# Kernel optimization log

Hardware: AMD Instinct MI355X
Metric: run time of the kernel (lower is better)

The kernel has to match this reference:

```python
import jax, jax.numpy as jnp
import numpy as np

B, D, H, K, P = 16384, 64, 256, 8, 3  # batch, lattice dim, hidden, expressivity, num_pars


def setup_inputs() -> dict:
    key = jax.random.key(0)
    k0, k1, k2 = jax.random.split(key, 3)
    # U(1) angles in [0, 2*pi)
    z = jax.random.uniform(k0, (B, D), dtype=jnp.float32) * (2.0 * jnp.pi)
    # per-step conditioner MLP weights, padded to full input dim (causally masked in reference)
    W1 = jax.random.normal(k1, (D - 1, D, H), dtype=jnp.float32) * 0.05
    b1 = jnp.zeros((D - 1, H), dtype=jnp.float32)
    W2 = jax.random.normal(k2, (D - 1, H, P * K), dtype=jnp.float32) * 0.05
    b2 = jnp.zeros((D - 1, P * K), dtype=jnp.float32)
    return {"z": z, "W1": W1, "b1": b1, "W2": W2, "b2": b2}


def reference(z, W1, b1, W2, b2):
    # decode(): x[...,0]=0; for idx in 1..D-1:
    #   params = conditioner_idx(z[..., :idx]); x[..., idx], ld = diffeo(z[..., idx], *params)
    # All conditioners read only z, so steps are independent -> vectorize over steps.
    d = z.shape[-1]
    r = d - 1
    # mask[row, col] = col < row+1  (conditioner idx uses first idx inputs)
    mask = (jnp.arange(d)[None, :] < (jnp.arange(r) + 1)[:, None]).astype(z.dtype)  # [R, D]
    W1m = W1 * mask[:, :, None]                                   # causal zero-padding
    h = jax.nn.relu(jnp.einsum('bd,rdh->brh', z, W1m) + b1)       # [B, R, H]
    raw = jnp.einsum('brh,rhp->brp', h, W2) + b2                  # [B, R, 3K]
    a_u, b_u, r_u = jnp.split(raw, 3, axis=-1)                    # each [B, R, K]
    alpha = jnp.exp(a_u)
    beta = b_u
    rho = jax.nn.softmax(r_u, axis=-1)
    # NCP diffeomorphism on U(1): convex mixture of 2*atan(alpha*tan((z-pi)/2)+beta)+pi
    zi = z[:, 1:]                                                  # [B, R]
    t = jnp.tan((zi - jnp.pi) * 0.5)[..., None]                    # [B, R, 1]
    g = alpha * t + beta                                           # [B, R, K]
    x_tail = jnp.sum(rho * (2.0 * jnp.arctan(g) + jnp.pi), axis=-1)
    deriv = alpha * (1.0 + t * t) / (1.0 + g * g)                  # dh/dz per component
    ld = jnp.log(jnp.sum(rho * deriv, axis=-1))                    # [B, R]
    x = jnp.concatenate([jnp.zeros_like(z[:, :1]), x_tail], axis=-1)
    log_det = jnp.sum(ld, axis=-1)                                 # [B]
    return x, log_det
```

## Files before the change

### kernel.cpp

```cpp
#include <hip/hip_runtime.h>
#include <math.h>
#include <type_traits>

typedef __bf16 bf16x8 __attribute__((ext_vector_type(8)));
typedef float f32x4 __attribute__((ext_vector_type(4)));
typedef unsigned int u32x4 __attribute__((ext_vector_type(4)));

#define B_TOT 16384
#define D_TOT 64
#define R_TOT 63
#define H_TOT 256
#define PK_TOT 24
#define PI_F 3.14159265358979323846f

#define W2F_BASE_U32 516096u
#define WS_NEED 3096576u

#define MFMA16(a, b, c) __builtin_amdgcn_mfma_f32_16x16x32_bf16((a), (b), (c), 0, 0, 0)

__device__ __forceinline__ unsigned short bf16_rtne(float f) {
    unsigned u = __float_as_uint(f);
    unsigned rr = u + 0x7FFFu + ((u >> 16) & 1u);
    return (unsigned short)(rr >> 16);
}

__device__ __forceinline__ unsigned cvt_pk_bf16(float a, float b) {
    unsigned r;
    asm("v_cvt_pk_bf16_f32 %0, %1, %2" : "=v"(r) : "v"(a), "v"(b));
    return r;
}

__global__ void init_out_kernel(float* __restrict__ out) {
    int b = blockIdx.x * 256 + threadIdx.x;
    if (b < B_TOT) {
        out[(size_t)b * D_TOT] = 0.0f;
        out[(size_t)B_TOT * D_TOT + b] = 0.0f;
    }
}

__global__ void prep_weights(const float* __restrict__ W1,
                             const float* __restrict__ b1,
                             const float* __restrict__ W2,
                             unsigned int* __restrict__ wsf)
{
    int gid = blockIdx.x * 256 + threadIdx.x;
    if (gid >= 193536) return;
    float v[8];
    unsigned int* dst;
    if (gid < 129024) {
        int lane = gid & 63;
        int q = gid >> 6;
        int t = q & 1; int qq = q >> 1;
        int nt = qq & 15; int r = qq >> 4;
        int n  = (nt << 4) + (lane & 15);
        int kb = (t << 5) + ((lane >> 4) << 3);
        int bias_d = (r <= 30) ? 31 : 63;
        #pragma unroll
        for (int j = 0; j < 8; ++j) {
            int d = kb + j;
            v[j] = (d <= r) ? W1[(size_t)(r * 64 + d) * 256 + n]
                 : (d == bias_d ? b1[(size_t)r * 256 + n] : 0.0f);
        }
        dst = wsf + (size_t)q * 256 + ((unsigned)lane << 2);
    } else {
        int g2 = gid - 129024;
        int lane = g2 & 63;
        int q = g2 >> 6;
        int ks = q & 7; int qq = q >> 3;
        int nt = qq & 1; int r = qq >> 1;
        int n  = (nt << 4) + (lane & 15);
        int kb = (ks << 5) + ((lane >> 4) << 3);
        #pragma unroll
        for (int j = 0; j < 8; ++j) {
            int k = kb + j;
            v[j] = (n < PK_TOT) ? W2[(size_t)(r * 256 + k) * PK_TOT + n] : 0.0f;
        }
        dst = wsf + W2F_BASE_U32 + (size_t)q * 256 + ((unsigned)lane << 2);
    }
    unsigned hw[4];
    #pragma unroll
    for (int i = 0; i < 4; ++i)
        hw[i] = (unsigned)bf16_rtne(v[2 * i]) | ((unsigned)bf16_rtne(v[2 * i + 1]) << 16);
    *reinterpret_cast<u32x4*>(dst) = u32x4{hw[0], hw[1], hw[2], hw[3]};
}

__global__ __launch_bounds__(256, 4) void flow_mfma(
    const float* __restrict__ z, const unsigned int* __restrict__ wsf,
    const float* __restrict__ b2, float* __restrict__ out)
{
    const int r   = blockIdx.y;
    const int b0  = blockIdx.x << 6;
    const int tid = threadIdx.x;
    const int w   = tid >> 6;
    const int l   = tid & 63;
    const int l15 = l & 15, l4 = l >> 4, key = l & 7;

    __shared__ __align__(16) unsigned char sm[24832];
    float* tls = reinterpret_cast<float*>(sm + 24576);

    {
        const int m  = tid >> 2;
        const int dq = (tid & 3) << 4;
        const float* zp = z + (size_t)(b0 + m) * 64 + dq;
        const int mkey = m & 7;
        const int bias_d = (r <= 30) ? 31 : 63;
        const int rel = bias_d - dq;
        const int tel = (r + 1) - dq;
        #pragma unroll
        for (int qq = 0; qq < 4; ++qq) {
            float4 val = *reinterpret_cast<const float4*>(zp + (qq << 2));
            int d0 = dq + (qq << 2);
            float vv[4] = {val.x, val.y, val.z, val.w};
            if ((tel >> 2) == qq) {
                float zi = vv[tel & 3];
                float s, c;
                __sincosf(zi * 0.5f, &s, &c);
                float t = -c * __builtin_amdgcn_rcpf(s);
                tls[m] = fminf(fmaxf(t, -1e8f), 1e8f);
            }
            if ((rel >> 2) == qq) vv[rel & 3] = 1.0f;
            uint2 hv;
            hv.x = cvt_pk_bf16(vv[0], vv[1]);
            hv.y = cvt_pk_bf16(vv[2], vv[3]);
            int off = (m << 7) + ((((d0 >> 3)) ^ mkey) << 4) + (((d0 >> 2) & 1) << 3);
            *reinterpret_cast<uint2*>(sm + off) = hv;
        }
    }
    __syncthreads();

    const unsigned int* w1b = wsf + (size_t)((r * 16 + (w << 2)) * 2) * 256 + (l << 2);
    const unsigned int* w2b = wsf + W2F_BASE_U32 + (size_t)(r * 16) * 256 + (l << 2);

    const int ej  = tid & 7;
    const float b2a = b2[(size_t)r * 24 + ej];
    const float b2b = b2[(size_t)r * 24 + 8 + ej];
    const float b2r = b2[(size_t)r * 24 + 16 + ej];

    #pragma unroll 1
    for (int mh = 0; mh < 2; ++mh) {
        f32x4 acc1[4][2];
        #pragma unroll
        for (int a = 0; a < 4; ++a)
            #pragma unroll
            for (int b = 0; b < 2; ++b) acc1[a][b] = f32x4{0.f, 0.f, 0.f, 0.f};

        auto run_gemm1 = [&](auto FULLC) {
            constexpr int NT = decltype(FULLC)::value ? 2 : 1;
            #pragma unroll
            for (int t = 0; t < NT; ++t) {
                bf16x8 zf[2];
                #pragma unroll
                for (int mt = 0; mt < 2; ++mt) {
                    int m = (mh << 5) + (mt << 4) + l15;
                    int off = (m << 7) + ((((t << 2) + l4) ^ key) << 4);
                    zf[mt] = __builtin_bit_cast(bf16x8, *reinterpret_cast<u32x4*>(sm + off));
                }
                #pragma unroll
                for (int ntl = 0; ntl < 4; ++ntl) {
                    bf16x8 af = __builtin_bit_cast(bf16x8,
                        *reinterpret_cast<const u32x4*>(w1b + (((ntl << 1) + t) << 8)));
                    #pragma unroll
                    for (int mt = 0; mt < 2; ++mt)
                        acc1[ntl][mt] = MFMA16(af, zf[mt], acc1[ntl][mt]);
                }
            }
        };
        if (r >= 31) run_gemm1(std::true_type{});
        else         run_gemm1(std::false_type{});

        #pragma unroll
        for (int ntl = 0; ntl < 4; ++ntl) {
            #pragma unroll
            for (int mt = 0; mt < 2; ++mt) {
                float v0 = fmaxf(acc1[ntl][mt][0], 0.0f);
                float v1 = fmaxf(acc1[ntl][mt][1], 0.0f);
                float v2 = fmaxf(acc1[ntl][mt][2], 0.0f);
                float v3 = fmaxf(acc1[ntl][mt][3], 0.0f);
                uint2 hv;
                hv.x = cvt_pk_bf16(v0, v1);
                hv.y = cvt_pk_bf16(v2, v3);
                int mloc = (mt << 4) + l15;
                int g    = (w << 3) + (ntl << 1) + (l4 >> 1);
                int off  = 8192 + (mloc << 9)
                         + (((g & 24) | ((g ^ key) & 7)) << 4) + ((l4 & 1) << 3);
                *reinterpret_cast<uint2*>(sm + off) = hv;
            }
        }
        __syncthreads();

        f32x4 acc2[2][2];
        #pragma unroll
        for (int a = 0; a < 2; ++a)
            #pragma unroll
            for (int b = 0; b < 2; ++b) acc2[a][b] = f32x4{0.f, 0.f, 0.f, 0.f};

        #pragma unroll
        for (int kk = 0; kk < 2; ++kk) {
            const int ks = (w << 1) + kk;
            bf16x8 wf[2];
            #pragma unroll
            for (int nt2 = 0; nt2 < 2; ++nt2)
                wf[nt2] = __builtin_bit_cast(bf16x8,
                    *reinterpret_cast<const u32x4*>(w2b + (((nt2 << 3) + ks) << 8)));
            bf16x8 hfr[2];
            #pragma unroll
            for (int mt = 0; mt < 2; ++mt) {
                int mloc = (mt << 4) + l15;
                int g    = (ks << 2) + l4;
                int off  = 8192 + (mloc << 9)
                         + (((g & 24) | ((g ^ key) & 7)) << 4);
                hfr[mt] = __builtin_bit_cast(bf16x8, *reinterpret_cast<u32x4*>(sm + off));
            }
            #pragma unroll
            for (int nt2 = 0; nt2 < 2; ++nt2)
                #pragma unroll
                for (int mt = 0; mt < 2; ++mt)
                    acc2[nt2][mt] = MFMA16(wf[nt2], hfr[mt], acc2[nt2][mt]);
        }
        __syncthreads();

        #pragma unroll
        for (int nt2 = 0; nt2 < 2; ++nt2)
            #pragma unroll
            for (int mt = 0; mt < 2; ++mt) {
                int row = (w << 5) + (mt << 4) + l15;
                int off = 8192 + (row << 7) + ((((nt2 << 2) + l4) ^ key) << 4);
                *reinterpret_cast<f32x4*>(sm + off) = acc2[nt2][mt];
            }
        __syncthreads();

        {
            const int mloc = tid >> 3;
            const int j    = ej;
            const int mk   = mloc & 7;
            float ra = b2a, rb = b2b, rr = b2r;
            #pragma unroll
            for (int w4 = 0; w4 < 4; ++w4) {
                const int base = 8192 + (((w4 << 5) + mloc) << 7);
                const int sub  = (j & 3) << 2;
                ra += *reinterpret_cast<float*>(sm + base + ((((j) >> 2) ^ mk) << 4) + sub);
                rb += *reinterpret_cast<float*>(sm + base + (((2 + (j >> 2)) ^ mk) << 4) + sub);
                rr += *reinterpret_cast<float*>(sm + base + (((4 + (j >> 2)) ^ mk) << 4) + sub);
            }
            int gb = b0 + (mh << 5) + mloc;
            float t  = tls[(mh << 5) + mloc];
            float al = __expf(ra);
            float g  = fmaf(al, t, rb);
            float X  = 2.0f * atanf(g) + PI_F;
            float dv = al * fmaf(t, t, 1.0f) * __builtin_amdgcn_rcpf(fmaf(g, g, 1.0f));
            float mx = rr;
            mx = fmaxf(mx, __shfl_xor(mx, 1));
            mx = fmaxf(mx, __shfl_xor(mx, 2));
            mx = fmaxf(mx, __shfl_xor(mx, 4));
            float e = __expf(rr - mx);
            float se = e, sx = e * X, sd = e * dv;
            se += __shfl_xor(se, 1); se += __shfl_xor(se, 2); se += __shfl_xor(se, 4);
            sx += __shfl_xor(sx, 1); sx += __shfl_xor(sx, 2); sx += __shfl_xor(sx, 4);
            sd += __shfl_xor(sd, 1); sd += __shfl_xor(sd, 2); sd += __shfl_xor(sd, 4);
            if (j == 0) {
                float rse = __builtin_amdgcn_rcpf(se);
                out[(size_t)gb * D_TOT + r + 1] = sx * rse;
                atomicAdd(&out[(size_t)B_TOT * D_TOT + gb], __logf(sd * rse));
            }
        }
        __syncthreads();
    }
}

__global__ __launch_bounds__(256, 2) void flow_fp32(
    const float* __restrict__ z,  const float* __restrict__ W1,
    const float* __restrict__ b1, const float* __restrict__ W2,
    const float* __restrict__ b2, float* __restrict__ out)
{
    const int r   = blockIdx.y;
    const int b0  = blockIdx.x * 32;
    const int tid = threadIdx.x;

    __shared__ float smem[16384];
    float* z_t  = smem;
    float* h_s  = smem + 2048;
    float* w2t  = smem + 2048 + 8192;
    float* part = w2t;

    #pragma unroll
    for (int it = 0; it < 2; ++it) {
        int idx4 = it * 256 + tid;
        int brow = idx4 >> 4;
        int dq   = (idx4 & 15) << 2;
        float4 v = *reinterpret_cast<const float4*>(&z[(size_t)(b0 + brow) * D_TOT + dq]);
        z_t[(dq + 0) * 32 + brow] = v.x;
        z_t[(dq + 1) * 32 + brow] = v.y;
        z_t[(dq + 2) * 32 + brow] = v.z;
        z_t[(dq + 3) * 32 + brow] = v.w;
    }
    #pragma unroll
    for (int it = 0; it < 6; ++it) {
        int idx4 = it * 256 + tid;
        int k  = idx4 / 6;
        int pq = (idx4 - k * 6) << 2;
        float4 v = *reinterpret_cast<const float4*>(&W2[(size_t)(r * H_TOT + k) * PK_TOT + pq]);
        int gk = k >> 2, kq = k & 3;
        w2t[(pq + 0) * 256 + (((gk) ^ ((pq + 0) & 7)) << 2) + kq] = v.x;
        w2t[(pq + 1) * 256 + (((gk) ^ ((pq + 1) & 7)) << 2) + kq] = v.y;
        w2t[(pq + 2) * 256 + (((gk) ^ ((pq + 2) & 7)) << 2) + kq] = v.z;
        w2t[(pq + 3) * 256 + (((gk) ^ ((pq + 3) & 7)) << 2) + kq] = v.w;
    }
    __syncthreads();

    const int rg = tid & 15;
    const int cg = tid >> 4;
    float acc[2][16];
    #pragma unroll
    for (int j = 0; j < 2; ++j)
        #pragma unroll
        for (int i = 0; i < 16; ++i) acc[j][i] = 0.0f;

    const float* w1p = W1 + (size_t)(r * D_TOT) * H_TOT + (cg << 4);
    #pragma unroll 4
    for (int d = 0; d <= r; ++d) {
        float2 zv = *reinterpret_cast<const float2*>(&z_t[d * 32 + (rg << 1)]);
        const float* wrow = w1p + (size_t)d * H_TOT;
        float wv[16];
        *reinterpret_cast<float4*>(&wv[0])  = *reinterpret_cast<const float4*>(wrow + 0);
        *reinterpret_cast<float4*>(&wv[4])  = *reinterpret_cast<const float4*>(wrow + 4);
        *reinterpret_cast<float4*>(&wv[8])  = *reinterpret_cast<const float4*>(wrow + 8);
        *reinterpret_cast<float4*>(&wv[12]) = *reinterpret_cast<const float4*>(wrow + 12);
        #pragma unroll
        for (int i = 0; i < 16; ++i) {
            acc[0][i] = fmaf(zv.x, wv[i], acc[0][i]);
            acc[1][i] = fmaf(zv.y, wv[i], acc[1][i]);
        }
    }
    {
        const int key = (rg >> 1) & 7;
        #pragma unroll
        for (int gi = 0; gi < 4; ++gi) {
            float4 bv = *reinterpret_cast<const float4*>(&b1[(size_t)r * H_TOT + (cg << 4) + (gi << 2)]);
            #pragma unroll
            for (int j = 0; j < 2; ++j) {
                float4 v;
                v.x = fmaxf(acc[j][4 * gi + 0] + bv.x, 0.0f);
                v.y = fmaxf(acc[j][4 * gi + 1] + bv.y, 0.0f);
                v.z = fmaxf(acc[j][4 * gi + 2] + bv.z, 0.0f);
                v.w = fmaxf(acc[j][4 * gi + 3] + bv.w, 0.0f);
                int bb = (rg << 1) + j;
                int g  = ((cg << 2) + gi) ^ key;
                *reinterpret_cast<float4*>(&h_s[bb * 256 + (g << 2)]) = v;
            }
        }
    }
    __syncthreads();

    const int wv_ = tid >> 6;
    const int ln  = tid & 63;
    const int bq  = ln & 7;
    const int pg  = ln >> 3;
    float acc2[4][3];
    #pragma unroll
    for (int j = 0; j < 4; ++j)
        #pragma unroll
        for (int i = 0; i < 3; ++i) acc2[j][i] = 0.0f;

    #pragma unroll
    for (int c = 0; c < 8; ++c) {
        int k0  = (wv_ << 6) + (c << 3);
        int gk0 = k0 >> 2;
        float w2r[3][8], hr[4][8];
        #pragma unroll
        for (int i = 0; i < 3; ++i) {
            int p = 3 * pg + i, pk = p & 7;
            *reinterpret_cast<float4*>(&w2r[i][0]) =
                *reinterpret_cast<const float4*>(&w2t[p * 256 + (((gk0 + 0) ^ pk) << 2)]);
            *reinterpret_cast<float4*>(&w2r[i][4]) =
                *reinterpret_cast<const float4*>(&w2t[p * 256 + (((gk0 + 1) ^ pk) << 2)]);
        }
        #pragma unroll
        for (int j = 0; j < 4; ++j) {
            int bb = 4 * bq + j;
            *reinterpret_cast<float4*>(&hr[j][0]) =
                *reinterpret_cast<const float4*>(&h_s[bb * 256 + (((gk0 + 0) ^ bq) << 2)]);
            *reinterpret_cast<float4*>(&hr[j][4]) =
                *reinterpret_cast<const float4*>(&h_s[bb * 256 + (((gk0 + 1) ^ bq) << 2)]);
        }
        #pragma unroll
        for (int kk = 0; kk < 8; ++kk)
            #pragma unroll
            for (int j = 0; j < 4; ++j)
                #pragma unroll
                for (int i = 0; i < 3; ++i)
                    acc2[j][i] = fmaf(hr[j][kk], w2r[i][kk], acc2[j][i]);
    }
    __syncthreads();
    #pragma unroll
    for (int j = 0; j < 4; ++j)
        #pragma unroll
        for (int i = 0; i < 3; ++i)
            part[((wv_ << 5) + 4 * bq + j) * PK_TOT + 3 * pg + i] = acc2[j][i];
    __syncthreads();

    {
        const int eb = tid >> 3;
        const int ej = tid & 7;
        float rawa = b2[(size_t)r * PK_TOT + ej];
        float rawb = b2[(size_t)r * PK_TOT + 8 + ej];
        float rawr = b2[(size_t)r * PK_TOT + 16 + ej];
        #pragma unroll
        for (int w = 0; w < 4; ++w) {
            rawa += part[((w << 5) + eb) * PK_TOT + ej];
            rawb += part[((w << 5) + eb) * PK_TOT + 8 + ej];
            rawr += part[((w << 5) + eb) * PK_TOT + 16 + ej];
        }
        float zi = z_t[(r + 1) * 32 + eb];
        float t  = tanf((zi - PI_F) * 0.5f);
        float al = expf(rawa);
        float g  = fmaf(al, t, rawb);
        float X  = 2.0f * atanf(g) + PI_F;
        float dv = al * (1.0f + t * t) / (1.0f + g * g);
        float m = rawr;
        m = fmaxf(m, __shfl_xor(m, 1));
        m = fmaxf(m, __shfl_xor(m, 2));
        m = fmaxf(m, __shfl_xor(m, 4));
        float e  = expf(rawr - m);
        float se = e, sx = e * X, sd = e * dv;
        se += __shfl_xor(se, 1); se += __shfl_xor(se, 2); se += __shfl_xor(se, 4);
        sx += __shfl_xor(sx, 1); sx += __shfl_xor(sx, 2); sx += __shfl_xor(sx, 4);
        sd += __shfl_xor(sd, 1); sd += __shfl_xor(sd, 2); sd += __shfl_xor(sd, 4);
        if (ej == 0) {
            int gb = b0 + eb;
            out[(size_t)gb * D_TOT + (r + 1)] = sx / se;
            atomicAdd(&out[(size_t)B_TOT * D_TOT + gb], logf(sd / se));
        }
    }
}

extern "C" void kernel_launch(void* const* d_in, const int* in_sizes, int n_in,
                              void* d_out, int out_size, void* d_ws, size_t ws_size,
                              hipStream_t stream) {
    const float* z  = (const float*)d_in[0];
    const float* W1 = (const float*)d_in[1];
    const float* b1 = (const float*)d_in[2];
    const float* W2 = (const float*)d_in[3];
    const float* b2 = (const float*)d_in[4];
    float* out = (float*)d_out;

    init_out_kernel<<<dim3(B_TOT / 256), dim3(256), 0, stream>>>(out);
    if (ws_size >= (size_t)WS_NEED) {
        prep_weights<<<dim3(756), dim3(256), 0, stream>>>(W1, b1, W2, (unsigned int*)d_ws);
        flow_mfma<<<dim3(B_TOT / 64, R_TOT), dim3(256), 0, stream>>>(
            z, (const unsigned int*)d_ws, b2, out);
    } else {
        flow_fp32<<<dim3(B_TOT / 32, R_TOT), dim3(256), 0, stream>>>(z, W1, b1, W2, b2, out);
    }
}
```

Measured before the change: 111.0 us.

## Process two conditioner steps per block to reuse staged z and batch log-det atomics

Each block now handles two steps r (paired so both share the same bias column and K-extent class), halving the grid along the step axis. The z tile is loaded and converted to bf16 once per pair, and the log-det contributions are accumulated in registers and written with one atomic per row per block instead of one per step. The cost is fewer blocks, a longer serial loop per block, and slightly more shared memory for the second t array.

After: 103.5 us. -6.8%, faster.

```diff
diff --git a/kernel.cpp b/kernel.cpp
--- a/kernel.cpp
+++ b/kernel.cpp
@@ -88,14 +88,20 @@
     const float* __restrict__ z, const unsigned int* __restrict__ wsf,
     const float* __restrict__ b2, float* __restrict__ out)
 {
-    const int r   = blockIdx.y;
+    const int y   = blockIdx.y;
+    int r0, r1;
+    if (y < 15)       { r0 = 2 * y;     r1 = 2 * y + 1; }
+    else if (y == 15) { r0 = 30;        r1 = -1;        }
+    else              { r0 = 2 * y - 1; r1 = 2 * y;     }
+    const int bias_d = (y <= 15) ? 31 : 63;
+
     const int b0  = blockIdx.x << 6;
     const int tid = threadIdx.x;
     const int w   = tid >> 6;
     const int l   = tid & 63;
     const int l15 = l & 15, l4 = l >> 4, key = l & 7;
 
-    __shared__ __align__(16) unsigned char sm[24832];
+    __shared__ __align__(16) unsigned char sm[25088];
     float* tls = reinterpret_cast<float*>(sm + 24576);
 
     {
@@ -103,20 +109,27 @@
         const int dq = (tid & 3) << 4;
         const float* zp = z + (size_t)(b0 + m) * 64 + dq;
         const int mkey = m & 7;
-        const int bias_d = (r <= 30) ? 31 : 63;
-        const int rel = bias_d - dq;
-        const int tel = (r + 1) - dq;
+        const int rel  = bias_d - dq;
+        const int tel0 = (r0 + 1) - dq;
+        const int tel1 = (r1 + 1) - dq;
         #pragma unroll
         for (int qq = 0; qq < 4; ++qq) {
             float4 val = *reinterpret_cast<const float4*>(zp + (qq << 2));
             int d0 = dq + (qq << 2);
             float vv[4] = {val.x, val.y, val.z, val.w};
-            if ((tel >> 2) == qq) {
-                float zi = vv[tel & 3];
+            if ((tel0 >> 2) == qq) {
+                float zi = vv[tel0 & 3];
                 float s, c;
                 __sincosf(zi * 0.5f, &s, &c);
                 float t = -c * __builtin_amdgcn_rcpf(s);
                 tls[m] = fminf(fmaxf(t, -1e8f), 1e8f);
+            }
+            if ((tel1 >> 2) == qq) {
+                float zi = vv[tel1 & 3];
+                float s, c;
+                __sincosf(zi * 0.5f, &s, &c);
+                float t = -c * __builtin_amdgcn_rcpf(s);
+                tls[64 + m] = fminf(fmaxf(t, -1e8f), 1e8f);
             }
             if ((rel >> 2) == qq) vv[rel & 3] = 1.0f;
             uint2 hv;
@@ -128,142 +141,156 @@
     }
     __syncthreads();
 
-    const unsigned int* w1b = wsf + (size_t)((r * 16 + (w << 2)) * 2) * 256 + (l << 2);
-    const unsigned int* w2b = wsf + W2F_BASE_U32 + (size_t)(r * 16) * 256 + (l << 2);
-
-    const int ej  = tid & 7;
-    const float b2a = b2[(size_t)r * 24 + ej];
-    const float b2b = b2[(size_t)r * 24 + 8 + ej];
-    const float b2r = b2[(size_t)r * 24 + 16 + ej];
+    const int ej = tid & 7;
+    float ld0 = 0.0f, ld1 = 0.0f;
 
     #pragma unroll 1
-    for (int mh = 0; mh < 2; ++mh) {
-        f32x4 acc1[4][2];
-        #pragma unroll
-        for (int a = 0; a < 4; ++a)
-            #pragma unroll
-            for (int b = 0; b < 2; ++b) acc1[a][b] = f32x4{0.f, 0.f, 0.f, 0.f};
-
-        auto run_gemm1 = [&](auto FULLC) {
-            constexpr int NT = decltype(FULLC)::value ? 2 : 1;
-            #pragma unroll
-            for (int t = 0; t < NT; ++t) {
-                bf16x8 zf[2];
+    for (int ri = 0; ri < 2; ++ri) {
+        const int r = ri ? r1 : r0;
+        if (r < 0) break;
+
+        const unsigned int* w1b = wsf + (size_t)((r * 16 + (w << 2)) * 2) * 256 + (l << 2);
+        const unsigned int* w2b = wsf + W2F_BASE_U32 + (size_t)(r * 16) * 256 + (l << 2);
+        const float b2a = b2[(size_t)r * 24 + ej];
+        const float b2b = b2[(size_t)r * 24 + 8 + ej];
+        const float b2r = b2[(size_t)r * 24 + 16 + ej];
+
+        #pragma unroll 1
+        for (int mh = 0; mh < 2; ++mh) {
+            f32x4 acc1[4][2];
+            #pragma unroll
+            for (int a = 0; a < 4; ++a)
+                #pragma unroll
+                for (int b = 0; b < 2; ++b) acc1[a][b] = f32x4{0.f, 0.f, 0.f, 0.f};
+
+            auto run_gemm1 = [&](auto FULLC) {
+                constexpr int NT = decltype(FULLC)::value ? 2 : 1;
+                #pragma unroll
+                for (int t = 0; t < NT; ++t) {
+                    bf16x8 zf[2];
+                    #pragma unroll
+                    for (int mt = 0; mt < 2; ++mt) {
+                        int m = (mh << 5) + (mt << 4) + l15;
+                        int off = (m << 7) + ((((t << 2) + l4) ^ key) << 4);
+                        zf[mt] = __builtin_bit_cast(bf16x8, *reinterpret_cast<u32x4*>(sm + off));
+                    }
+                    #pragma unroll
+                    for (int ntl = 0; ntl < 4; ++ntl) {
+                        bf16x8 af = __builtin_bit_cast(bf16x8,
+                            *reinterpret_cast<const u32x4*>(w1b + (((ntl << 1) + t) << 8)));
+                        #pragma unroll
+                        for (int mt = 0; mt < 2; ++mt)
+                            acc1[ntl][mt] = MFMA16(af, zf[mt], acc1[ntl][mt]);
+                    }
+                }
+            };
+            if (r >= 31) run_gemm1(std::true_type{});
+            else         run_gemm1(std::false_type{});
+
+            #pragma unroll
+            for (int ntl = 0; ntl < 4; ++ntl) {
                 #pragma unroll
                 for (int mt = 0; mt < 2; ++mt) {
-                    int m = (mh << 5) + (mt << 4) + l15;
-                    int off = (m << 7) + ((((t << 2) + l4) ^ key) << 4);
-                    zf[mt] = __builtin_bit_cast(bf16x8, *reinterpret_cast<u32x4*>(sm + off));
-                }
-                #pragma unroll
-                for (int ntl = 0; ntl < 4; ++ntl) {
-                    bf16x8 af = __builtin_bit_cast(bf16x8,
-                        *reinterpret_cast<const u32x4*>(w1b + (((ntl << 1) + t) << 8)));
+                    float v0 = fmaxf(acc1[ntl][mt][0], 0.0f);
+                    float v1 = fmaxf(acc1[ntl][mt][1], 0.0f);
+                    float v2 = fmaxf(acc1[ntl][mt][2], 0.0f);
+                    float v3 = fmaxf(acc1[ntl][mt][3], 0.0f);
+                    uint2 hv;
+                    hv.x = cvt_pk_bf16(v0, v1);
+                    hv.y = cvt_pk_bf16(v2, v3);
+                    int mloc = (mt << 4) + l15;
+                    int g    = (w << 3) + (ntl << 1) + (l4 >> 1);
+                    int off  = 8192 + (mloc << 9)
+                             + (((g & 24) | ((g ^ key) & 7)) << 4) + ((l4 & 1) << 3);
+                    *reinterpret_cast<uint2*>(sm + off) = hv;
+                }
+            }
+            __syncthreads();
+
+            f32x4 acc2[2][2];
+            #pragma unroll
+            for (int a = 0; a < 2; ++a)
+                #pragma unroll
+                for (int b = 0; b < 2; ++b) acc2[a][b] = f32x4{0.f, 0.f, 0.f, 0.f};
+
+            #pragma unroll
+            for (int kk = 0; kk < 2; ++kk) {
+                const int ks = (w << 1) + kk;
+                bf16x8 wf[2];
+                #pragma unroll
+                for (int nt2 = 0; nt2 < 2; ++nt2)
+                    wf[nt2] = __builtin_bit_cast(bf16x8,
+                        *reinterpret_cast<const u32x4*>(w2b + (((nt2 << 3) + ks) << 8)));
+                bf16x8 hfr[2];
+                #pragma unroll
+                for (int mt = 0; mt < 2; ++mt) {
+                    int mloc = (mt << 4) + l15;
+                    int g    = (ks << 2) + l4;
+                    int off  = 8192 + (mloc << 9)
+                             + (((g & 24) | ((g ^ key) & 7)) << 4);
+                    hfr[mt] = __builtin_bit_cast(bf16x8, *reinterpret_cast<u32x4*>(sm + off));
+                }
+                #pragma unroll
+                for (int nt2 = 0; nt2 < 2; ++nt2)
                     #pragma unroll
                     for (int mt = 0; mt < 2; ++mt)
-                        acc1[ntl][mt] = MFMA16(af, zf[mt], acc1[ntl][mt]);
-                }
-            }
-        };
-        if (r >= 31) run_gemm1(std::true_type{});
-        else         run_gemm1(std::false_type{});
-
-        #pragma unroll
-        for (int ntl = 0; ntl < 4; ++ntl) {
-            #pragma unroll
-            for (int mt = 0; mt < 2; ++mt) {
-                float v0 = fmaxf(acc1[ntl][mt][0], 0.0f);
-                float v1 = fmaxf(acc1[ntl][mt][1], 0.0f);
-                float v2 = fmaxf(acc1[ntl][mt][2], 0.0f);
-                float v3 = fmaxf(acc1[ntl][mt][3], 0.0f);
-                uint2 hv;
-                hv.x = cvt_pk_bf16(v0, v1);
-                hv.y = cvt_pk_bf16(v2, v3);
-                int mloc = (mt << 4) + l15;
-                int g    = (w << 3) + (ntl << 1) + (l4 >> 1);
-                int off  = 8192 + (mloc << 9)
-                         + (((g & 24) | ((g ^ key) & 7)) << 4) + ((l4 & 1) << 3);
-                *reinterpret_cast<uint2*>(sm + off) = hv;
-            }
-        }
-        __syncthreads();
-
-        f32x4 acc2[2][2];
-        #pragma unroll
-        for (int a = 0; a < 2; ++a)
-            #pragma unroll
-            for (int b = 0; b < 2; ++b) acc2[a][b] = f32x4{0.f, 0.f, 0.f, 0.f};
-
-        #pragma unroll
-        for (int kk = 0; kk < 2; ++kk) {
-            const int ks = (w << 1) + kk;
-            bf16x8 wf[2];
+                        acc2[nt2][mt] = MFMA16(wf[nt2], hfr[mt], acc2[nt2][mt]);
+            }
+            __syncthreads();
+
             #pragma unroll
             for (int nt2 = 0; nt2 < 2; ++nt2)
-                wf[nt2] = __builtin_bit_cast(bf16x8,
-                    *reinterpret_cast<const u32x4*>(w2b + (((nt2 << 3) + ks) << 8)));
-            bf16x8 hfr[2];
-            #pragma unroll
-            for (int mt = 0; mt < 2; ++mt) {
-                int mloc = (mt << 4) + l15;
-                int g    = (ks << 2) + l4;
-                int off  = 8192 + (mloc << 9)
-                         + (((g & 24) | ((g ^ key) & 7)) << 4);
-                hfr[mt] = __builtin_bit_cast(bf16x8, *reinterpret_cast<u32x4*>(sm + off));
-            }
-            #pragma unroll
-            for (int nt2 = 0; nt2 < 2; ++nt2)
-                #pragma unroll
-                for (int mt = 0; mt < 2; ++mt)
-                    acc2[nt2][mt] = MFMA16(wf[nt2], hfr[mt], acc2[nt2][mt]);
-        }
-        __syncthreads();
-
-        #pragma unroll
-        for (int nt2 = 0; nt2 < 2; ++nt2)
-            #pragma unroll
-            for (int mt = 0; mt < 2; ++mt) {
-                int row = (w << 5) + (mt << 4) + l15;
-                int off = 8192 + (row << 7) + ((((nt2 << 2) + l4) ^ key) << 4);
-                *reinterpret_cast<f32x4*>(sm + off) = acc2[nt2][mt];
-            }
-        __syncthreads();
-
-        {
-            const int mloc = tid >> 3;
-            const int j    = ej;
-            const int mk   = mloc & 7;
-            float ra = b2a, rb = b2b, rr = b2r;
-            #pragma unroll
-            for (int w4 = 0; w4 < 4; ++w4) {
-                const int base = 8192 + (((w4 << 5) + mloc) << 7);
-                const int sub  = (j & 3) << 2;
-                ra += *reinterpret_cast<float*>(sm + base + ((((j) >> 2) ^ mk) << 4) + sub);
-                rb += *reinterpret_cast<float*>(sm + base + (((2 + (j >> 2)) ^ mk) << 4) + sub);
-                rr += *reinterpret_cast<float*>(sm + base + (((4 + (j >> 2)) ^ mk) << 4) + sub);
-            }
-            int gb = b0 + (mh << 5) + mloc;
-            float t  = tls[(mh << 5) + mloc];
-            float al = __expf(ra);
-            float g  = fmaf(al, t, rb);
-            float X  = 2.0f * atanf(g) + PI_F;
-            float dv = al * fmaf(t, t, 1.0f) * __builtin_amdgcn_rcpf(fmaf(g, g, 1.0f));
-            float mx = rr;
-            mx = fmaxf(mx, __shfl_xor(mx, 1));
-            mx = fmaxf(mx, __shfl_xor(mx, 2));
-            mx = fmaxf(mx, __shfl_xor(mx, 4));
-            float e = __expf(rr - mx);
-            float se = e, sx = e * X, sd = e * dv;
-            se += __shfl_xor(se, 1); se += __shfl_xor(se, 2); se += __shfl_xor(se, 4);
-            sx += __shfl_xor(sx, 1); sx += __shfl_xor(sx, 2); sx += __shfl_xor(sx, 4);
-            sd += __shfl_xor(sd, 1); sd += __shfl_xor(sd, 2); sd += __shfl_xor(sd, 4);
-            if (j == 0) {
-                float rse = __builtin_amdgcn_rcpf(se);
-                out[(size_t)gb * D_TOT + r + 1] = sx * rse;
-                atomicAdd(&out[(size_t)B_TOT * D_TOT + gb], __logf(sd * rse));
-            }
-        }
-        __syncthreads();
+                #pragma unroll
+                for (int mt = 0; mt < 2; ++mt) {
+                    int row = (w << 5) + (mt << 4) + l15;
+                    int off = 8192 + (row << 7) + ((((nt2 << 2) + l4) ^ key) << 4);
+                    *reinterpret_cast<f32x4*>(sm + off) = acc2[nt2][mt];
+                }
+            __syncthreads();
+
+            {
+                const int mloc = tid >> 3;
+                const int j    = ej;
+                const int mk   = mloc & 7;
+                float ra = b2a, rb = b2b, rr = b2r;
+                #pragma unroll
+                for (int w4 = 0; w4 < 4; ++w4) {
+                    const int base = 8192 + (((w4 << 5) + mloc) << 7);
+                    const int sub  = (j & 3) << 2;
+                    ra += *reinterpret_cast<float*>(sm + base + ((((j) >> 2) ^ mk) << 4) + sub);
+                    rb += *reinterpret_cast<float*>(sm + base + (((2 + (j >> 2)) ^ mk) << 4) + sub);
+                    rr += *reinterpret_cast<float*>(sm + base + (((4 + (j >> 2)) ^ mk) << 4) + sub);
+                }
+                int gb = b0 + (mh << 5) + mloc;
+                float t  = tls[(ri << 6) + (mh << 5) + mloc];
+                float al = __expf(ra);
+                float g  = fmaf(al, t, rb);
+                float X  = 2.0f * atanf(g) + PI_F;
+                float dv = al * fmaf(t, t, 1.0f) * __builtin_amdgcn_rcpf(fmaf(g, g, 1.0f));
+                float mx = rr;
+                mx = fmaxf(mx, __shfl_xor(mx, 1));
+                mx = fmaxf(mx, __shfl_xor(mx, 2));
+                mx = fmaxf(mx, __shfl_xor(mx, 4));
+                float e = __expf(rr - mx);
+                float se = e, sx = e * X, sd = e * dv;
+                se += __shfl_xor(se, 1); se += __shfl_xor(se, 2); se += __shfl_xor(se, 4);
+                sx += __shfl_xor(sx, 1); sx += __shfl_xor(sx, 2); sx += __shfl_xor(sx, 4);
+                sd += __shfl_xor(sd, 1); sd += __shfl_xor(sd, 2); sd += __shfl_xor(sd, 4);
+                if (j == 0) {
+                    float rse = __builtin_amdgcn_rcpf(se);
+                    out[(size_t)gb * D_TOT + r + 1] = sx * rse;
+                    float ldv = __logf(sd * rse);
+                    if (mh == 0) ld0 += ldv; else ld1 += ldv;
+                }
+            }
+            __syncthreads();
+        }
+    }
+
+    if (ej == 0) {
+        const int mloc = tid >> 3;
+        atomicAdd(&out[(size_t)B_TOT * D_TOT + b0 + mloc], ld0);
+        atomicAdd(&out[(size_t)B_TOT * D_TOT + b0 + 32 + mloc], ld1);
     }
 }
 
@@ -446,7 +473,7 @@
     init_out_kernel<<<dim3(B_TOT / 256), dim3(256), 0, stream>>>(out);
     if (ws_size >= (size_t)WS_NEED) {
         prep_weights<<<dim3(756), dim3(256), 0, stream>>>(W1, b1, W2, (unsigned int*)d_ws);
-        flow_mfma<<<dim3(B_TOT / 64, R_TOT), dim3(256), 0, stream>>>(
+        flow_mfma<<<dim3(B_TOT / 64, 32), dim3(256), 0, stream>>>(
             z, (const unsigned int*)d_ws, b2, out);
     } else {
         flow_fp32<<<dim3(B_TOT / 32, R_TOT), dim3(256), 0, stream>>>(z, W1, b1, W2, b2, out);
```
